# Performance work log

Hardware: AMD Instinct MI355X
Metric: run time of the kernel (lower is better)

The kernel has to match this reference:

```python
import jax, jax.numpy as jnp
import numpy as np

R = 64          # n_rois
B = 128         # batch_size (graphs)
IN = 2048       # voxels per ROI
HID = 512       # max(32, IN//4)
ROI_OUT = 20
G1, G2 = 64, 128
FC1, FC2, OUT = 512, 1024, 6400
N = R * B       # total graph nodes


def _block_complete_edges():
    # per-sample complete directed graph over R ROIs (no self loops)
    r = np.arange(R)
    s, d = np.meshgrid(r, r, indexing='ij')
    m = s != d
    s, d = s[m], d[m]                       # [R*(R-1)]
    off = (np.arange(B) * R)[:, None]       # [B,1]
    src = (s[None, :] + off).reshape(-1)
    dst = (d[None, :] + off).reshape(-1)
    return np.stack([src, dst]).astype(np.int64)  # [2, E]


def setup_inputs() -> dict:
    key = jax.random.key(0)
    ks = jax.random.split(key, 16)
    sd = lambda *s: 1.0 / np.sqrt(s[0])
    inp = {
        'x': jax.random.normal(ks[0], (R, B * IN), jnp.float32),
        'edge_index': jnp.asarray(_block_complete_edges()),
        'batch': jnp.repeat(jnp.arange(B, dtype=jnp.int64), R),
        # per-ROI MLP params (batched over ROI axis)
        'W1': jax.random.normal(ks[1], (R, IN, HID), jnp.float32) * sd(IN),
        'b1': jnp.zeros((R, HID), jnp.float32),
        'W2': jax.random.normal(ks[2], (R, HID, ROI_OUT), jnp.float32) * sd(HID),
        'b2': jnp.zeros((R, ROI_OUT), jnp.float32),
        # GCN params
        'Wg1': jax.random.normal(ks[3], (ROI_OUT, G1), jnp.float32) * sd(ROI_OUT),
        'bg1': jnp.zeros((G1,), jnp.float32),
        'Wg2': jax.random.normal(ks[4], (G1, G2), jnp.float32) * sd(G1),
        'bg2': jnp.zeros((G2,), jnp.float32),
        # FC stack
        'Wf1': jax.random.normal(ks[5], (G2, FC1), jnp.float32) * sd(G2),
        'bf1': jnp.zeros((FC1,), jnp.float32),
        'Wf2': jax.random.normal(ks[6], (FC1, FC2), jnp.float32) * sd(FC1),
        'bf2': jnp.zeros((FC2,), jnp.float32),
        'Wo': jax.random.normal(ks[7], (FC2, OUT), jnp.float32) * sd(FC2),
        'bo': jnp.zeros((OUT,), jnp.float32),
    }
    return inp


def _gcn(h, src, dst, W, b):
    # PyG GCNConv: symmetric norm with self loops, then linear
    loop = jnp.arange(N)
    s = jnp.concatenate([src, loop])
    d = jnp.concatenate([dst, loop])
    deg = jax.ops.segment_sum(jnp.ones(s.shape[0], h.dtype), d, num_segments=N)
    dinv = jax.lax.rsqrt(deg)  # deg >= 1 due to self loops
    hw = h @ W                                  # [N, out]
    msg = hw[s] * (dinv[s] * dinv[d])[:, None]  # [E+N, out]
    return jax.ops.segment_sum(msg, d, num_segments=N) + b


def reference(x, edge_index, batch, W1, b1, W2, b2, Wg1, bg1, Wg2, bg2,
              Wf1, bf1, Wf2, bf2, Wo, bo):
    # per-ROI MLPs, batched: x[r] holds B contiguous chunks of IN voxels
    xr = x.reshape(R, B, IN)
    h = jax.nn.relu(jnp.einsum('rbi,rih->rbh', xr, W1) + b1[:, None, :])
    f = jnp.einsum('rbh,rho->rbo', h, W2) + b2[:, None, :]   # [R,B,ROI_OUT]
    # node order in torch code: for b: for r -> node = b*R + r
    node_feats = f.transpose(1, 0, 2).reshape(N, ROI_OUT)

    src, dst = edge_index[0], edge_index[1]
    g = jax.nn.relu(_gcn(node_feats, src, dst, Wg1, bg1))
    g = jax.nn.relu(_gcn(g, src, dst, Wg2, bg2))

    # global mean pool over each graph's R nodes
    pooled = jax.ops.segment_sum(g, batch, num_segments=B) / R  # [B, G2]

    y = jax.nn.relu(pooled @ Wf1 + bf1)
    y = jax.nn.relu(y @ Wf2 + bf2)
    return y @ Wo + bo  # [B, OUT]
```

## Files before the change

### kernel.cpp

```cpp
#include <hip/hip_runtime.h>
#include <hip/hip_bf16.h>
#include <cstdint>

typedef float  f32x4 __attribute__((ext_vector_type(4)));
typedef short  s16x4 __attribute__((ext_vector_type(4)));
typedef short  s16x8 __attribute__((ext_vector_type(8)));
typedef __bf16 bf16x8 __attribute__((ext_vector_type(8)));
typedef unsigned int u32x2 __attribute__((ext_vector_type(2)));
typedef unsigned int u32x4 __attribute__((ext_vector_type(4)));

static __device__ __forceinline__ unsigned short f2bf(float f) {
  union { float f; unsigned u; } v; v.f = f;
  unsigned r = v.u + 0x7fffu + ((v.u >> 16) & 1u);
  return (unsigned short)(r >> 16);
}

static __device__ __forceinline__ unsigned pk2(float lo, float hi) {
  unsigned r;
  asm("v_cvt_pk_bf16_f32 %0, %1, %2" : "=v"(r) : "v"(lo), "v"(hi));
  return r;
}

static __device__ __forceinline__ f32x4 mfma16(bf16x8 a, bf16x8 b, f32x4 c) {
  return __builtin_amdgcn_mfma_f32_16x16x32_bf16(a, b, c, 0, 0, 0);
}

__global__ __launch_bounds__(512)
void k_mlp(const float* __restrict__ X, const float* __restrict__ W1,
           const float* __restrict__ b1, const float* __restrict__ W2,
           float* __restrict__ m1)
{
  __shared__ short smem[21760];
  __shared__ float biasS[128];
  short* const lds_a  = smem;
  short* const lds_b  = smem + 9216;
  short* const lds_h  = smem;
  short* const lds_w2 = smem + 17408;

  const int bid = blockIdx.x;
  const int r = (bid & 7) + ((bid >> 5) << 3);
  const int c = (bid >> 3) & 3;

  const float* xr = X + (long)r * (128 * 2048);
  const float* wr = W1 + (long)r * (2048 * 512) + c * 128;
  const float* bp = b1 + (long)r * 512 + c * 128;

  const int t = threadIdx.x;
  const int lane = t & 63;
  const int w = t >> 6;

  if (t < 128) biasS[t] = bp[t];

  const int aRow = t >> 2;
  const int aCol = (t & 3) * 4;
  const int bn   = t & 127;
  const int bk0  = (t >> 7) * 8;

  f32x4 aR0[4], aR1[4];
  float bR0[2][8], bR1[2][8];

  auto loadTile = [&](int ks, f32x4 (&aS)[4], float (&bS)[2][8]) {
    const float* xp = xr + (long)aRow * 2048 + ks * 64 + aCol;
#pragma unroll
    for (int j = 0; j < 4; j++)
      aS[j] = *(const f32x4*)(xp + 16 * j);
    const float* wp = wr + (long)(ks * 64 + bk0) * 512 + bn;
#pragma unroll
    for (int g = 0; g < 2; g++)
#pragma unroll
      for (int j = 0; j < 8; j++)
        bS[g][j] = wp[(long)(g * 32 + j) * 512];
  };

  auto storeTile = [&](f32x4 (&aS)[4], float (&bS)[2][8]) {
#pragma unroll
    for (int j = 0; j < 4; j++) {
      u32x2 v;
      v[0] = pk2(aS[j][0], aS[j][1]);
      v[1] = pk2(aS[j][2], aS[j][3]);
      *(u32x2*)&lds_a[aRow * 72 + aCol + 16 * j] = v;
    }
#pragma unroll
    for (int g = 0; g < 2; g++) {
      u32x4 v;
      v[0] = pk2(bS[g][0], bS[g][1]);
      v[1] = pk2(bS[g][2], bS[g][3]);
      v[2] = pk2(bS[g][4], bS[g][5]);
      v[3] = pk2(bS[g][6], bS[g][7]);
      *(u32x4*)&lds_b[bn * 72 + bk0 + g * 32] = v;
    }
  };

  const int wm = w & 1, wn = w >> 1;
  const int mBase = wm * 64, nBase = wn * 32;
  const int lm = lane & 15, lg = lane >> 4;

  f32x4 acc[4][2];
#pragma unroll
  for (int i = 0; i < 4; i++)
#pragma unroll
    for (int j = 0; j < 2; j++) acc[i][j] = f32x4{0.f, 0.f, 0.f, 0.f};

  auto compute = [&]() {
    bf16x8 af[2][4], bfr[2][2];
#pragma unroll
    for (int g = 0; g < 2; g++) {
#pragma unroll
      for (int i = 0; i < 4; i++)
        af[g][i] = *(const bf16x8*)&lds_a[(mBase + i * 16 + lm) * 72 + g * 32 + lg * 8];
#pragma unroll
      for (int j = 0; j < 2; j++)
        bfr[g][j] = *(const bf16x8*)&lds_b[(nBase + j * 16 + lm) * 72 + g * 32 + lg * 8];
    }
#pragma unroll
    for (int mi = 0; mi < 4; mi++)
#pragma unroll
      for (int ni = 0; ni < 2; ni++) {
        acc[mi][ni] = mfma16(af[0][mi], bfr[0][ni], acc[mi][ni]);
        acc[mi][ni] = mfma16(af[1][mi], bfr[1][ni], acc[mi][ni]);
      }
  };

  loadTile(0, aR0, bR0);
  loadTile(1, aR1, bR1);
  for (int ks = 0; ks < 32; ks += 2) {
    __syncthreads();
    storeTile(aR0, bR0);
    __syncthreads();
    if (ks + 2 < 32) loadTile(ks + 2, aR0, bR0);
    compute();
    __syncthreads();
    storeTile(aR1, bR1);
    __syncthreads();
    if (ks + 3 < 32) loadTile(ks + 3, aR1, bR1);
    compute();
  }

  __syncthreads();

#pragma unroll
  for (int mi = 0; mi < 4; mi++)
#pragma unroll
    for (int ni = 0; ni < 2; ni++) {
      const int col = nBase + ni * 16 + lm;
      const float bv = biasS[col];
#pragma unroll
      for (int i = 0; i < 4; i++) {
        const int row = mBase + mi * 16 + lg * 4 + i;
        float v = acc[mi][ni][i] + bv;
        v = v > 0.f ? v : 0.f;
        lds_h[row * 136 + col] = (short)f2bf(v);
      }
    }
  {
    const float* w2r = W2 + (long)r * (512 * 20) + (long)(c * 128) * 20;
#pragma unroll
    for (int i = 0; i < 8; i++) {
      const int idx = t * 8 + i;
      const int o = idx >> 7, kh = idx & 127;
      const float v = (o < 20) ? w2r[(long)kh * 20 + o] : 0.f;
      lds_w2[o * 136 + kh] = (short)f2bf(v);
    }
  }
  __syncthreads();
  f32x4 acc2[2];
  acc2[0] = f32x4{0.f, 0.f, 0.f, 0.f};
  acc2[1] = f32x4{0.f, 0.f, 0.f, 0.f};
#pragma unroll
  for (int ks2 = 0; ks2 < 4; ks2++) {
    bf16x8 a0 = *(const bf16x8*)&lds_h[(w * 16 + lm) * 136 + ks2 * 32 + lg * 8];
    bf16x8 b0 = *(const bf16x8*)&lds_w2[lm * 136 + ks2 * 32 + lg * 8];
    bf16x8 b1v = *(const bf16x8*)&lds_w2[(16 + lm) * 136 + ks2 * 32 + lg * 8];
    acc2[0] = mfma16(a0, b0, acc2[0]);
    acc2[1] = mfma16(a0, b1v, acc2[1]);
  }
#pragma unroll
  for (int ni = 0; ni < 2; ni++)
#pragma unroll
    for (int i = 0; i < 4; i++) {
      const int m = w * 16 + lg * 4 + i;
      const int o = ni * 16 + lm;
      if (o < 20)
        atomicAdd(&m1[m * 20 + o], acc2[ni][i] * (1.f / 64.f));
    }
}

template<int RELU>
__global__ __launch_bounds__(256)
void gemm_n64(const float* __restrict__ X, int ldx,
              const float* __restrict__ W, int ldw,
              const float* __restrict__ bias,
              float* __restrict__ out, int ldo, int kSteps)
{
  __shared__ short lds_a[128 * 72];
  __shared__ short lds_b[64 * 72];
  __shared__ float biasS[64];

  const int c = blockIdx.x;
  const int t = threadIdx.x;
  const int lane = t & 63;
  const int w = t >> 6;

  if (t < 64) biasS[t] = bias[c * 64 + t];

  const int aRow = t >> 2;
  const int aCol = (t & 3) * 4;
  const int bn   = t & 63;
  const int bk0  = w * 8;

  f32x4 aR[2][4];
  float bR[2][8];

  auto loadTile = [&](int ks) {
    const float* xp = X + (long)aRow * ldx + ks * 64 + aCol;
#pragma unroll
    for (int j = 0; j < 4; j++) {
      aR[0][j] = *(const f32x4*)(xp + 16 * j);
      aR[1][j] = *(const f32x4*)(xp + (long)64 * ldx + 16 * j);
    }
    const float* wp = W + (long)(ks * 64 + bk0) * ldw + c * 64 + bn;
#pragma unroll
    for (int g = 0; g < 2; g++)
#pragma unroll
      for (int j = 0; j < 8; j++)
        bR[g][j] = wp[(long)(g * 32 + j) * ldw];
  };

  auto storeTile = [&]() {
#pragma unroll
    for (int g = 0; g < 2; g++)
#pragma unroll
      for (int j = 0; j < 4; j++) {
        u32x2 v;
        v[0] = pk2(aR[g][j][0], aR[g][j][1]);
        v[1] = pk2(aR[g][j][2], aR[g][j][3]);
        *(u32x2*)&lds_a[(aRow + 64 * g) * 72 + aCol + 16 * j] = v;
      }
#pragma unroll
    for (int g = 0; g < 2; g++) {
      u32x4 v;
      v[0] = pk2(bR[g][0], bR[g][1]);
      v[1] = pk2(bR[g][2], bR[g][3]);
      v[2] = pk2(bR[g][4], bR[g][5]);
      v[3] = pk2(bR[g][6], bR[g][7]);
      *(u32x4*)&lds_b[bn * 72 + bk0 + g * 32] = v;
    }
  };

  const int wm = w & 1, wn = w >> 1;
  const int mBase = wm * 64, nBase = wn * 32;
  const int lm = lane & 15, lg = lane >> 4;

  f32x4 acc[4][2];
#pragma unroll
  for (int i = 0; i < 4; i++)
#pragma unroll
    for (int j = 0; j < 2; j++) acc[i][j] = f32x4{0.f, 0.f, 0.f, 0.f};

  loadTile(0);
  for (int ks = 0; ks < kSteps; ks++) {
    __syncthreads();
    storeTile();
    __syncthreads();
    if (ks + 1 < kSteps) loadTile(ks + 1);
    bf16x8 af[2][4], bfr[2][2];
#pragma unroll
    for (int g = 0; g < 2; g++) {
#pragma unroll
      for (int i = 0; i < 4; i++)
        af[g][i] = *(const bf16x8*)&lds_a[(mBase + i * 16 + lm) * 72 + g * 32 + lg * 8];
#pragma unroll
      for (int j = 0; j < 2; j++)
        bfr[g][j] = *(const bf16x8*)&lds_b[(nBase + j * 16 + lm) * 72 + g * 32 + lg * 8];
    }
#pragma unroll
    for (int mi = 0; mi < 4; mi++)
#pragma unroll
      for (int ni = 0; ni < 2; ni++) {
        acc[mi][ni] = mfma16(af[0][mi], bfr[0][ni], acc[mi][ni]);
        acc[mi][ni] = mfma16(af[1][mi], bfr[1][ni], acc[mi][ni]);
      }
  }

  float* outp = out + c * 64;
#pragma unroll
  for (int mi = 0; mi < 4; mi++)
#pragma unroll
    for (int ni = 0; ni < 2; ni++) {
      const int col = nBase + ni * 16 + lm;
      const float bv = biasS[col];
#pragma unroll
      for (int i = 0; i < 4; i++) {
        const int row = mBase + mi * 16 + lg * 4 + i;
        float v = acc[mi][ni][i] + bv;
        if (RELU) v = v > 0.f ? v : 0.f;
        outp[(long)row * ldo + col] = v;
      }
    }
}

__global__ void k_init_m1(const float* __restrict__ b2, float* __restrict__ m1) {
  const int i = blockIdx.x * blockDim.x + threadIdx.x;
  if (i >= 128 * 20) return;
  const int o = i % 20;
  float s = 0.f;
  for (int r = 0; r < 64; r++) s += b2[r * 20 + o];
  m1[i] = s * (1.f / 64.f);
}

template<int K, int RELU>
__global__ void k_fc_small(const float* __restrict__ in, const float* __restrict__ Wt,
                           const float* __restrict__ bias, float* __restrict__ out,
                           int N)
{
  const int i = blockIdx.x * blockDim.x + threadIdx.x;
  const int b = i / N;
  if (b >= 128) return;
  const int j = i - b * N;
  float s = bias[j];
  const float* ip = in + (long)b * K;
#pragma unroll
  for (int k = 0; k < K; k++) s += ip[k] * Wt[k * N + j];
  out[i] = (RELU && s < 0.f) ? 0.f : s;
}

extern "C" void kernel_launch(void* const* d_in, const int* in_sizes, int n_in,
                              void* d_out, int out_size, void* d_ws, size_t ws_size,
                              hipStream_t stream)
{
  const float* x   = (const float*)d_in[0];
  const float* W1  = (const float*)d_in[3];
  const float* b1  = (const float*)d_in[4];
  const float* W2  = (const float*)d_in[5];
  const float* b2  = (const float*)d_in[6];
  const float* Wg1 = (const float*)d_in[7];
  const float* bg1 = (const float*)d_in[8];
  const float* Wg2 = (const float*)d_in[9];
  const float* bg2 = (const float*)d_in[10];
  const float* Wf1 = (const float*)d_in[11];
  const float* bf1 = (const float*)d_in[12];
  const float* Wf2 = (const float*)d_in[13];
  const float* bf2 = (const float*)d_in[14];
  const float* Wo  = (const float*)d_in[15];
  const float* bo  = (const float*)d_in[16];
  float* out = (float*)d_out;

  float* ws = (float*)d_ws;
  float* m1 = ws;
  float* g1 = ws + 4096;
  float* g2 = ws + 16384;
  float* y1 = ws + 32768;
  float* y2 = ws + 98304;

  k_init_m1<<<10, 256, 0, stream>>>(b2, m1);
  k_mlp<<<256, 512, 0, stream>>>(x, W1, b1, W2, m1);
  k_fc_small<20, 1><<<32, 256, 0, stream>>>(m1, Wg1, bg1, g1, 64);
  k_fc_small<64, 1><<<64, 256, 0, stream>>>(g1, Wg2, bg2, g2, 128);
  gemm_n64<1><<<8,   256, 0, stream>>>(g2, 128,  Wf1, 512,  bf1, y1, 512, 2);
  gemm_n64<1><<<16,  256, 0, stream>>>(y1, 512,  Wf2, 1024, bf2, y2, 1024, 8);
  gemm_n64<0><<<100, 256, 0, stream>>>(y2, 1024, Wo,  6400, bo,  out, 6400, 16);
}
```

Measured before the change: 495.6 us.

## Vectorize W1 tile loads and replace atomic m1 accumulation with partial-sum reduction

```diff
diff --git a/kernel.cpp b/kernel.cpp
--- a/kernel.cpp
+++ b/kernel.cpp
@@ -28,7 +28,7 @@
 __global__ __launch_bounds__(512)
 void k_mlp(const float* __restrict__ X, const float* __restrict__ W1,
            const float* __restrict__ b1, const float* __restrict__ W2,
-           float* __restrict__ m1)
+           float* __restrict__ m1part)
 {
   __shared__ short smem[21760];
   __shared__ float biasS[128];
@@ -53,26 +53,27 @@
 
   const int aRow = t >> 2;
   const int aCol = (t & 3) * 4;
-  const int bn   = t & 127;
-  const int bk0  = (t >> 7) * 8;
+  const int kq = t & 31;
+  const int ng = t >> 5;
+  const int k0 = kq * 2;
+  const int n0 = ng * 8;
 
   f32x4 aR0[4], aR1[4];
-  float bR0[2][8], bR1[2][8];
-
-  auto loadTile = [&](int ks, f32x4 (&aS)[4], float (&bS)[2][8]) {
+  f32x4 bR0[4], bR1[4];
+
+  auto loadTile = [&](int ks, f32x4 (&aS)[4], f32x4 (&bS)[4]) {
     const float* xp = xr + (long)aRow * 2048 + ks * 64 + aCol;
 #pragma unroll
     for (int j = 0; j < 4; j++)
       aS[j] = *(const f32x4*)(xp + 16 * j);
-    const float* wp = wr + (long)(ks * 64 + bk0) * 512 + bn;
-#pragma unroll
-    for (int g = 0; g < 2; g++)
-#pragma unroll
-      for (int j = 0; j < 8; j++)
-        bS[g][j] = wp[(long)(g * 32 + j) * 512];
-  };
-
-  auto storeTile = [&](f32x4 (&aS)[4], float (&bS)[2][8]) {
+    const float* wp = wr + (long)(ks * 64 + k0) * 512 + n0;
+    bS[0] = *(const f32x4*)(wp);
+    bS[1] = *(const f32x4*)(wp + 4);
+    bS[2] = *(const f32x4*)(wp + 512);
+    bS[3] = *(const f32x4*)(wp + 516);
+  };
+
+  auto storeTile = [&](f32x4 (&aS)[4], f32x4 (&bS)[4]) {
 #pragma unroll
     for (int j = 0; j < 4; j++) {
       u32x2 v;
@@ -81,14 +82,11 @@
       *(u32x2*)&lds_a[aRow * 72 + aCol + 16 * j] = v;
     }
 #pragma unroll
-    for (int g = 0; g < 2; g++) {
-      u32x4 v;
-      v[0] = pk2(bS[g][0], bS[g][1]);
-      v[1] = pk2(bS[g][2], bS[g][3]);
-      v[2] = pk2(bS[g][4], bS[g][5]);
-      v[3] = pk2(bS[g][6], bS[g][7]);
-      *(u32x4*)&lds_b[bn * 72 + bk0 + g * 32] = v;
-    }
+    for (int j = 0; j < 4; j++)
+      *(unsigned*)&lds_b[(n0 + j) * 72 + k0] = pk2(bS[0][j], bS[2][j]);
+#pragma unroll
+    for (int j = 0; j < 4; j++)
+      *(unsigned*)&lds_b[(n0 + 4 + j) * 72 + k0] = pk2(bS[1][j], bS[3][j]);
   };
 
   const int wm = w & 1, wn = w >> 1;
@@ -174,15 +172,33 @@
     acc2[0] = mfma16(a0, b0, acc2[0]);
     acc2[1] = mfma16(a0, b1v, acc2[1]);
   }
-#pragma unroll
-  for (int ni = 0; ni < 2; ni++)
-#pragma unroll
-    for (int i = 0; i < 4; i++) {
-      const int m = w * 16 + lg * 4 + i;
-      const int o = ni * 16 + lm;
-      if (o < 20)
-        atomicAdd(&m1[m * 20 + o], acc2[ni][i] * (1.f / 64.f));
-    }
+  {
+    float* pout = m1part + (long)bid * 2560;
+#pragma unroll
+    for (int ni = 0; ni < 2; ni++)
+#pragma unroll
+      for (int i = 0; i < 4; i++) {
+        const int m = w * 16 + lg * 4 + i;
+        const int o = ni * 16 + lm;
+        if (o < 20)
+          pout[m * 20 + o] = acc2[ni][i];
+      }
+  }
+}
+
+__global__ void k_reduce_m1(const float* __restrict__ part,
+                            const float* __restrict__ b2,
+                            float* __restrict__ m1)
+{
+  const int i = blockIdx.x * blockDim.x + threadIdx.x;
+  if (i >= 128 * 20) return;
+  const int o = i % 20;
+  float s = 0.f;
+#pragma unroll 8
+  for (int r = 0; r < 64; r++) s += b2[r * 20 + o];
+#pragma unroll 8
+  for (int p = 0; p < 256; p++) s += part[(long)p * 2560 + i];
+  m1[i] = s * (1.f / 64.f);
 }
 
 template<int RELU>
@@ -297,15 +313,6 @@
         outp[(long)row * ldo + col] = v;
       }
     }
-}
-
-__global__ void k_init_m1(const float* __restrict__ b2, float* __restrict__ m1) {
-  const int i = blockIdx.x * blockDim.x + threadIdx.x;
-  if (i >= 128 * 20) return;
-  const int o = i % 20;
-  float s = 0.f;
-  for (int r = 0; r < 64; r++) s += b2[r * 20 + o];
-  m1[i] = s * (1.f / 64.f);
 }
 
 template<int K, int RELU>
@@ -351,9 +358,10 @@
   float* g2 = ws + 16384;
   float* y1 = ws + 32768;
   float* y2 = ws + 98304;
-
-  k_init_m1<<<10, 256, 0, stream>>>(b2, m1);
-  k_mlp<<<256, 512, 0, stream>>>(x, W1, b1, W2, m1);
+  float* m1part = ws + 262144;
+
+  k_mlp<<<256, 512, 0, stream>>>(x, W1, b1, W2, m1part);
+  k_reduce_m1<<<10, 256, 0, stream>>>(m1part, b2, m1);
   k_fc_small<20, 1><<<32, 256, 0, stream>>>(m1, Wg1, bg1, g1, 64);
   k_fc_small<64, 1><<<64, 256, 0, stream>>>(g1, Wg2, bg2, g2, 128);
   gemm_n64<1><<<8,   256, 0, stream>>>(g2, 128,  Wf1, 512,  bf1, y1, 512, 2);
```

New measurement: 503.7 us. Within noise of the previous version (+1.6%).
